# Performance work log

Measured on AMD Instinct MI355X. Metric: run time of the kernel, lower is better.

## Reference

```python
import jax, jax.numpy as jnp
from jax import lax
import numpy as np

WINDOW_SIZE = 11
SIGMA = 1.5
C1 = 0.01 ** 2
C2 = 0.03 ** 2


def _gauss_1d(n=WINDOW_SIZE, sigma=SIGMA):
    # replicates cv2.getGaussianKernel(n, sigma)
    x = np.arange(n, dtype=np.float64) - (n - 1) / 2.0
    g = np.exp(-(x ** 2) / (2.0 * sigma ** 2))
    return (g / g.sum()).astype(np.float32)


def _blur(x, g):
    """Separable 2D Gaussian blur of x [N,1,H,W]; math equals conv with g g^T."""
    p = g.shape[0] // 2
    kh = g.reshape(1, 1, -1, 1).astype(x.dtype)  # [O,I,KH,1]
    kw = g.reshape(1, 1, 1, -1).astype(x.dtype)  # [O,I,1,KW]
    dn = ('NCHW', 'OIHW', 'NCHW')
    x = lax.conv_general_dilated(x, kh, (1, 1), [(p, p), (0, 0)], dimension_numbers=dn)
    x = lax.conv_general_dilated(x, kw, (1, 1), [(0, 0), (p, p)], dimension_numbers=dn)
    return x


def _ssim_loss_2d(a, b):
    """a, b: [N,1,H,W]. Returns 1 - mean(SSIM map) with the module's exact formula."""
    g = jnp.asarray(_gauss_1d())
    mu1 = _blur(a, g)
    mu2 = _blur(b, g)
    mu1_sq = mu1 * mu1
    mu2_sq = mu2 * mu2
    mu1_mu2 = mu1 * mu2
    sigma1_sq = _blur(a * a, g) - mu1_sq
    sigma2_sq = _blur(b * b, g) - mu2_sq
    sigma12 = _blur(a * b, g) - mu1_mu2
    luminance = (2 * mu1_mu2 + C1) / (mu1_sq + mu2_sq + C1)
    contrast = (2 * sigma12 + C2) / (sigma1_sq + sigma2_sq + C2)
    structure = (sigma12 + C2) / (jnp.sqrt(sigma1_sq) * jnp.sqrt(sigma2_sq) + C2)
    ssim = luminance * contrast * structure
    return 1.0 - ssim.mean()


def setup_inputs() -> dict:
    key = jax.random.key(0)
    k1, k2, k3 = jax.random.split(key, 3)
    img1_3d = jax.random.uniform(k1, (4, 1, 16, 512, 512), dtype=jnp.float32)
    img1_2d = jax.random.uniform(k2, (4, 1, 512, 512), dtype=jnp.float32)
    img2 = jax.random.uniform(k3, (4, 1, 16, 512, 512), dtype=jnp.float32)
    return {"img1_3d": img1_3d, "img1_2d": img1_2d, "img2": img2}


def reference(img1_3d, img1_2d, img2):
    B, C, D, H, W = img1_3d.shape  # C == 1 (forced by groups=C with single-out-channel weight)
    # 3D SSIM: kernel depth 1, depth padding 0 -> per-slice 2D blur; fold D into batch.
    a3 = img1_3d.reshape(B * D, 1, H, W)
    b3 = img2.reshape(B * D, 1, H, W)
    loss3d = _ssim_loss_2d(a3, b3)
    # 2D SSIM against depth-averaged img2.
    b2 = jnp.mean(img2, axis=2)  # [B,1,H,W]
    loss2d = _ssim_loss_2d(img1_2d, b2)
    return loss3d + loss2d
```

## Files before the change

kernel.cpp:

```cpp
#include <hip/hip_runtime.h>
#include <cmath>


#define WSZ 11
#define IMG 512
#define SLICE (IMG * IMG)

typedef float f32x2 __attribute__((ext_vector_type(2)));
typedef float f32x4 __attribute__((ext_vector_type(4)));

struct G11 { float w[WSZ]; };

__device__ __forceinline__ void row_barrier()
{
    asm volatile("s_waitcnt lgkmcnt(0)" ::: "memory");
    __builtin_amdgcn_s_barrier();
}

__global__ __launch_bounds__(256, 4)
void ssim_pk_kernel(const float* __restrict__ A3, const float* __restrict__ B3,
                    const float* __restrict__ A2, const float* __restrict__ B2,
                    double* __restrict__ acc, G11 gw)
{
    __shared__ f32x4 A4[4][262];
    __shared__ f32x4 B4[4][262];
    __shared__ f32x2 Z2[4][262];
    __shared__ float bsum[4];

    const int tx = threadIdx.x;
    const int x0 = tx * 2;

    const int unit = blockIdx.x;
    const float* Ap;
    const float* Bp;
    double* accp;
    int y0, BAND;
    if (unit < 1024) {
        int slice = unit >> 4;
        int band  = unit & 15;
        Ap = A3 + (long)slice * SLICE;
        Bp = B3 + (long)slice * SLICE;
        accp = acc + 0;
        y0 = band * 32;
        BAND = 32;
    } else {
        int uu = unit - 1024;
        int img  = uu >> 6;
        int band = uu & 63;
        Ap = A2 + (long)img * SLICE;
        Bp = B2 + (long)img * SLICE;
        accp = acc + 1;
        y0 = band * 8;
        BAND = 8;
    }
    const int ITER = BAND >> 1;

    if (tx < 3) {
        f32x4 z4 = {0.f, 0.f, 0.f, 0.f};
        f32x2 z2 = {0.f, 0.f};
        #pragma unroll
        for (int b = 0; b < 4; b++) {
            A4[b][tx] = z4; A4[b][259 + tx] = z4;
            B4[b][tx] = z4; B4[b][259 + tx] = z4;
            Z2[b][tx] = z2; Z2[b][259 + tx] = z2;
        }
    }

    f32x2 ra[12], rb[12];

    float sum = 0.f;
    const f32x2 C1v = {1e-4f, 1e-4f};
    const f32x2 C2v = {9e-4f, 9e-4f};

    #pragma unroll
    for (int t = 0; t < 10; t++) {
        int r = y0 - 5 + t;
        f32x2 a = {0.f, 0.f}, b = {0.f, 0.f};
        if (r >= 0) {
            a = *(const f32x2*)&Ap[(long)r * IMG + x0];
            b = *(const f32x2*)&Bp[(long)r * IMG + x0];
        }
        ra[t] = a; rb[t] = b;
    }
    ra[10] = (f32x2){0.f, 0.f}; rb[10] = (f32x2){0.f, 0.f};
    ra[11] = (f32x2){0.f, 0.f}; rb[11] = (f32x2){0.f, 0.f};

    f32x2 aN0 = {0.f, 0.f}, bN0 = aN0, aN1 = aN0, bN1 = aN0;
    {
        int r0 = y0 + 5, r1 = y0 + 6;
        if (r0 < IMG) { aN0 = *(const f32x2*)&Ap[(long)r0 * IMG + x0];
                        bN0 = *(const f32x2*)&Bp[(long)r0 * IMG + x0]; }
        if (r1 < IMG) { aN1 = *(const f32x2*)&Ap[(long)r1 * IMG + x0];
                        bN1 = *(const f32x2*)&Bp[(long)r1 * IMG + x0]; }
    }

    auto vpass = [&](int base, int buf) {
        f32x2 m1 = {0.f, 0.f}, m2 = m1, xx = m1, yy = m1, zz = m1;
        #pragma unroll
        for (int j = 0; j < 11; j++) {
            const int s = (base + j) % 12;
            const f32x2 g2 = {gw.w[j], gw.w[j]};
            f32x2 a = ra[s], b = rb[s];
            f32x2 ga = g2 * a, gb = g2 * b;
            m1 += ga; m2 += gb;
            xx += ga * a; yy += gb * b; zz += ga * b;
        }
        A4[buf][3 + tx] = __builtin_shufflevector(m1, m2, 0, 1, 2, 3);
        B4[buf][3 + tx] = __builtin_shufflevector(xx, yy, 0, 1, 2, 3);
        Z2[buf][3 + tx] = zz;
    };

    auto hpass = [&](int buf) {
        f32x2 OM1 = {0.f, 0.f}, OM2 = OM1, OXX = OM1, OYY = OM1, OZZ = OM1;
        {
            f32x4 pa = A4[buf][tx], pb = B4[buf][tx];
            f32x2 pz = Z2[buf][tx];
            const f32x2 c = {gw.w[0], 0.f};
            OM1 += c * __builtin_shufflevector(pa, pa, 1, 1);
            OM2 += c * __builtin_shufflevector(pa, pa, 3, 3);
            OXX += c * __builtin_shufflevector(pb, pb, 1, 1);
            OYY += c * __builtin_shufflevector(pb, pb, 3, 3);
            OZZ += c * __builtin_shufflevector(pz, pz, 1, 1);
        }
        #pragma unroll
        for (int jj = 1; jj <= 5; jj++) {
            f32x4 pa = A4[buf][tx + jj], pb = B4[buf][tx + jj];
            f32x2 pz = Z2[buf][tx + jj];
            const f32x2 cA = {gw.w[2 * jj - 1], gw.w[2 * jj - 2]};
            const f32x2 cB = {gw.w[2 * jj],     gw.w[2 * jj - 1]};
            OM1 += cA * __builtin_shufflevector(pa, pa, 0, 0)
                 + cB * __builtin_shufflevector(pa, pa, 1, 1);
            OM2 += cA * __builtin_shufflevector(pa, pa, 2, 2)
                 + cB * __builtin_shufflevector(pa, pa, 3, 3);
            OXX += cA * __builtin_shufflevector(pb, pb, 0, 0)
                 + cB * __builtin_shufflevector(pb, pb, 1, 1);
            OYY += cA * __builtin_shufflevector(pb, pb, 2, 2)
                 + cB * __builtin_shufflevector(pb, pb, 3, 3);
            OZZ += cA * __builtin_shufflevector(pz, pz, 0, 0)
                 + cB * __builtin_shufflevector(pz, pz, 1, 1);
        }
        {
            f32x4 pa = A4[buf][tx + 6], pb = B4[buf][tx + 6];
            f32x2 pz = Z2[buf][tx + 6];
            const f32x2 c = {0.f, gw.w[10]};
            OM1 += c * __builtin_shufflevector(pa, pa, 0, 0);
            OM2 += c * __builtin_shufflevector(pa, pa, 2, 2);
            OXX += c * __builtin_shufflevector(pb, pb, 0, 0);
            OYY += c * __builtin_shufflevector(pb, pb, 2, 2);
            OZZ += c * __builtin_shufflevector(pz, pz, 0, 0);
        }
        f32x2 m1s = OM1 * OM1, m2s = OM2 * OM2, m12 = OM1 * OM2;
        f32x2 s1 = OXX - m1s, s2 = OYY - m2s, s12 = OZZ - m12;
        f32x2 d1 = m1s + m2s + C1v;
        f32x2 d2 = s1 + s2 + C2v;
        f32x2 num = (2.f * m12 + C1v) * (2.f * s12 + C2v) * (s12 + C2v);
        float d3x = __builtin_amdgcn_sqrtf(s1.x) * __builtin_amdgcn_sqrtf(s2.x) + 9e-4f;
        float d3y = __builtin_amdgcn_sqrtf(s1.y) * __builtin_amdgcn_sqrtf(s2.y) + 9e-4f;
        sum += num.x * __builtin_amdgcn_rcpf(d1.x * d2.x * d3x);
        sum += num.y * __builtin_amdgcn_rcpf(d1.y * d2.y * d3y);
    };

    for (int kk = 0; kk < ITER; kk += 6) {
        #pragma unroll
        for (int u = 0; u < 6; u++) {
            const int k = kk + u;
            if (k < ITER) {
                const int s0 = (10 + 2 * u) % 12;
                const int s1 = (11 + 2 * u) % 12;
                ra[s0] = aN0; rb[s0] = bN0;
                ra[s1] = aN1; rb[s1] = bN1;

                {
                    int r0 = y0 + 7 + 2 * k, r1 = r0 + 1;
                    aN0 = (f32x2){0.f, 0.f}; bN0 = aN0; aN1 = aN0; bN1 = aN0;
                    if (k + 1 < ITER) {
                        if (r0 < IMG) { aN0 = *(const f32x2*)&Ap[(long)r0 * IMG + x0];
                                        bN0 = *(const f32x2*)&Bp[(long)r0 * IMG + x0]; }
                        if (r1 < IMG) { aN1 = *(const f32x2*)&Ap[(long)r1 * IMG + x0];
                                        bN1 = *(const f32x2*)&Bp[(long)r1 * IMG + x0]; }
                    }
                }

                const int b0 = (u & 1) * 2;
                vpass(2 * u,     b0);
                vpass(2 * u + 1, b0 + 1);
                row_barrier();
                hpass(b0);
                hpass(b0 + 1);
            }
        }
    }

    for (int off = 32; off > 0; off >>= 1)
        sum += __shfl_down(sum, off, 64);
    if ((tx & 63) == 0) bsum[tx >> 6] = sum;
    __syncthreads();
    if (tx == 0) {
        float tot = bsum[0] + bsum[1] + bsum[2] + bsum[3];
        atomicAdd(accp, (double)tot);
    }
}

__global__ __launch_bounds__(256) void depth_mean4_kernel(
    const float4* __restrict__ img2, float4* __restrict__ b2)
{
    const int per = SLICE / 4;
    int idx = blockIdx.x * 256 + threadIdx.x;
    int b = idx >> 16;
    int p = idx & (per - 1);
    const float4* src = img2 + (long)b * 16 * per + p;
    float sx = 0.f, sy = 0.f, sz = 0.f, sw = 0.f;
    #pragma unroll
    for (int d = 0; d < 16; d++) {
        float4 v = src[(long)d * per];
        sx += v.x; sy += v.y; sz += v.z; sw += v.w;
    }
    float4 o; o.x = sx * 0.0625f; o.y = sy * 0.0625f; o.z = sz * 0.0625f; o.w = sw * 0.0625f;
    b2[idx] = o;
}

__global__ void finalize_kernel(const double* __restrict__ acc, float* __restrict__ out)
{
    double loss3 = 1.0 - acc[0] / (64.0 * (double)SLICE);
    double loss2 = 1.0 - acc[1] / (4.0 * (double)SLICE);
    out[0] = (float)(loss3 + loss2);
}

extern "C" void kernel_launch(void* const* d_in, const int* in_sizes, int n_in,
                              void* d_out, int out_size, void* d_ws, size_t ws_size,
                              hipStream_t stream)
{
    const float* img1_3d = (const float*)d_in[0];
    const float* img1_2d = (const float*)d_in[1];
    const float* img2    = (const float*)d_in[2];
    float* out = (float*)d_out;

    double* acc = (double*)d_ws;
    float*  b2  = (float*)((char*)d_ws + 256);

    G11 gw;
    {
        double g[WSZ], s = 0.0;
        for (int i = 0; i < WSZ; i++) {
            double xx = (double)i - (WSZ - 1) / 2.0;
            g[i] = std::exp(-(xx * xx) / (2.0 * 1.5 * 1.5));
            s += g[i];
        }
        for (int i = 0; i < WSZ; i++) gw.w[i] = (float)(g[i] / s);
    }

    hipMemsetAsync(acc, 0, 2 * sizeof(double), stream);

    depth_mean4_kernel<<<(4 * SLICE / 4) / 256, 256, 0, stream>>>(
        (const float4*)img2, (float4*)b2);

    ssim_pk_kernel<<<1280, 256, 0, stream>>>(img1_3d, img2, img1_2d, b2, acc, gw);

    finalize_kernel<<<1, 1, 0, stream>>>(acc, out);
}
```

Baseline: 95.28 us.

## Reorder separable blur to horizontal-first with register ring of vertical accumulators

The kernel now writes raw input rows (a,b) into shared memory and applies the horizontal blur first, computing squares and products on the fly. Each horizontal result is scattered into an 11-slot register ring of vertical accumulators, and a row's SSIM is evaluated once its accumulator is complete. This cuts shared-memory traffic from five blurred quantities to two raw values per pixel. In exchange it recomputes products per tap, adds halo rows to the loop, and raises register pressure, so the occupancy hint drops from 4 to 3.

```diff
diff --git a/kernel.cpp b/kernel.cpp
--- a/kernel.cpp
+++ b/kernel.cpp
@@ -17,14 +17,12 @@
     __builtin_amdgcn_s_barrier();
 }
 
-__global__ __launch_bounds__(256, 4)
-void ssim_pk_kernel(const float* __restrict__ A3, const float* __restrict__ B3,
+__global__ __launch_bounds__(256, 3)
+void ssim_hf_kernel(const float* __restrict__ A3, const float* __restrict__ B3,
                     const float* __restrict__ A2, const float* __restrict__ B2,
                     double* __restrict__ acc, G11 gw)
 {
-    __shared__ f32x4 A4[4][262];
-    __shared__ f32x4 B4[4][262];
-    __shared__ f32x2 Z2[4][262];
+    __shared__ f32x4 R4[4][262];
     __shared__ float bsum[4];
 
     const int tx = threadIdx.x;
@@ -53,140 +51,134 @@
         y0 = band * 8;
         BAND = 8;
     }
-    const int ITER = BAND >> 1;
+    const int NPAIR = (BAND + 10) >> 1;
 
     if (tx < 3) {
         f32x4 z4 = {0.f, 0.f, 0.f, 0.f};
-        f32x2 z2 = {0.f, 0.f};
-        #pragma unroll
-        for (int b = 0; b < 4; b++) {
-            A4[b][tx] = z4; A4[b][259 + tx] = z4;
-            B4[b][tx] = z4; B4[b][259 + tx] = z4;
-            Z2[b][tx] = z2; Z2[b][259 + tx] = z2;
-        }
-    }
-
-    f32x2 ra[12], rb[12];
+        #pragma unroll
+        for (int b = 0; b < 4; b++) { R4[b][tx] = z4; R4[b][259 + tx] = z4; }
+    }
+
+    f32x2 aM1[11], aM2[11], aXX[11], aYY[11], aZZ[11];
+    #pragma unroll
+    for (int i = 0; i < 11; i++) {
+        aM1[i] = (f32x2){0.f, 0.f}; aM2[i] = aM1[i]; aXX[i] = aM1[i];
+        aYY[i] = aM1[i]; aZZ[i] = aM1[i];
+    }
 
     float sum = 0.f;
     const f32x2 C1v = {1e-4f, 1e-4f};
     const f32x2 C2v = {9e-4f, 9e-4f};
 
-    #pragma unroll
-    for (int t = 0; t < 10; t++) {
-        int r = y0 - 5 + t;
-        f32x2 a = {0.f, 0.f}, b = {0.f, 0.f};
-        if (r >= 0) {
-            a = *(const f32x2*)&Ap[(long)r * IMG + x0];
-            b = *(const f32x2*)&Bp[(long)r * IMG + x0];
-        }
-        ra[t] = a; rb[t] = b;
-    }
-    ra[10] = (f32x2){0.f, 0.f}; rb[10] = (f32x2){0.f, 0.f};
-    ra[11] = (f32x2){0.f, 0.f}; rb[11] = (f32x2){0.f, 0.f};
-
     f32x2 aN0 = {0.f, 0.f}, bN0 = aN0, aN1 = aN0, bN1 = aN0;
     {
-        int r0 = y0 + 5, r1 = y0 + 6;
-        if (r0 < IMG) { aN0 = *(const f32x2*)&Ap[(long)r0 * IMG + x0];
-                        bN0 = *(const f32x2*)&Bp[(long)r0 * IMG + x0]; }
-        if (r1 < IMG) { aN1 = *(const f32x2*)&Ap[(long)r1 * IMG + x0];
-                        bN1 = *(const f32x2*)&Bp[(long)r1 * IMG + x0]; }
-    }
-
-    auto vpass = [&](int base, int buf) {
-        f32x2 m1 = {0.f, 0.f}, m2 = m1, xx = m1, yy = m1, zz = m1;
-        #pragma unroll
-        for (int j = 0; j < 11; j++) {
-            const int s = (base + j) % 12;
-            const f32x2 g2 = {gw.w[j], gw.w[j]};
-            f32x2 a = ra[s], b = rb[s];
-            f32x2 ga = g2 * a, gb = g2 * b;
-            m1 += ga; m2 += gb;
-            xx += ga * a; yy += gb * b; zz += ga * b;
-        }
-        A4[buf][3 + tx] = __builtin_shufflevector(m1, m2, 0, 1, 2, 3);
-        B4[buf][3 + tx] = __builtin_shufflevector(xx, yy, 0, 1, 2, 3);
-        Z2[buf][3 + tx] = zz;
-    };
-
-    auto hpass = [&](int buf) {
-        f32x2 OM1 = {0.f, 0.f}, OM2 = OM1, OXX = OM1, OYY = OM1, OZZ = OM1;
+        int r0 = y0 - 5, r1 = y0 - 4;
+        if (r0 >= 0 && r0 < IMG) { aN0 = *(const f32x2*)&Ap[(long)r0 * IMG + x0];
+                                   bN0 = *(const f32x2*)&Bp[(long)r0 * IMG + x0]; }
+        if (r1 >= 0 && r1 < IMG) { aN1 = *(const f32x2*)&Ap[(long)r1 * IMG + x0];
+                                   bN1 = *(const f32x2*)&Bp[(long)r1 * IMG + x0]; }
+    }
+
+    auto PROC = [&](int set, int u2, bool complete) {
+        f32x2 H1 = {0.f, 0.f}, H2 = H1, H3 = H1, H4 = H1, H5 = H1;
         {
-            f32x4 pa = A4[buf][tx], pb = B4[buf][tx];
-            f32x2 pz = Z2[buf][tx];
+            f32x4 p = R4[set][tx];
+            f32x4 q = p * p;
+            f32x2 ab = __builtin_shufflevector(p, p, 0, 1)
+                     * __builtin_shufflevector(p, p, 2, 3);
             const f32x2 c = {gw.w[0], 0.f};
-            OM1 += c * __builtin_shufflevector(pa, pa, 1, 1);
-            OM2 += c * __builtin_shufflevector(pa, pa, 3, 3);
-            OXX += c * __builtin_shufflevector(pb, pb, 1, 1);
-            OYY += c * __builtin_shufflevector(pb, pb, 3, 3);
-            OZZ += c * __builtin_shufflevector(pz, pz, 1, 1);
+            H1 += c * __builtin_shufflevector(p, p, 1, 1);
+            H2 += c * __builtin_shufflevector(p, p, 3, 3);
+            H3 += c * __builtin_shufflevector(q, q, 1, 1);
+            H4 += c * __builtin_shufflevector(q, q, 3, 3);
+            H5 += c * __builtin_shufflevector(ab, ab, 1, 1);
         }
         #pragma unroll
         for (int jj = 1; jj <= 5; jj++) {
-            f32x4 pa = A4[buf][tx + jj], pb = B4[buf][tx + jj];
-            f32x2 pz = Z2[buf][tx + jj];
+            f32x4 p = R4[set][tx + jj];
+            f32x4 q = p * p;
+            f32x2 ab = __builtin_shufflevector(p, p, 0, 1)
+                     * __builtin_shufflevector(p, p, 2, 3);
             const f32x2 cA = {gw.w[2 * jj - 1], gw.w[2 * jj - 2]};
             const f32x2 cB = {gw.w[2 * jj],     gw.w[2 * jj - 1]};
-            OM1 += cA * __builtin_shufflevector(pa, pa, 0, 0)
-                 + cB * __builtin_shufflevector(pa, pa, 1, 1);
-            OM2 += cA * __builtin_shufflevector(pa, pa, 2, 2)
-                 + cB * __builtin_shufflevector(pa, pa, 3, 3);
-            OXX += cA * __builtin_shufflevector(pb, pb, 0, 0)
-                 + cB * __builtin_shufflevector(pb, pb, 1, 1);
-            OYY += cA * __builtin_shufflevector(pb, pb, 2, 2)
-                 + cB * __builtin_shufflevector(pb, pb, 3, 3);
-            OZZ += cA * __builtin_shufflevector(pz, pz, 0, 0)
-                 + cB * __builtin_shufflevector(pz, pz, 1, 1);
+            H1 += cA * __builtin_shufflevector(p, p, 0, 0)
+                + cB * __builtin_shufflevector(p, p, 1, 1);
+            H2 += cA * __builtin_shufflevector(p, p, 2, 2)
+                + cB * __builtin_shufflevector(p, p, 3, 3);
+            H3 += cA * __builtin_shufflevector(q, q, 0, 0)
+                + cB * __builtin_shufflevector(q, q, 1, 1);
+            H4 += cA * __builtin_shufflevector(q, q, 2, 2)
+                + cB * __builtin_shufflevector(q, q, 3, 3);
+            H5 += cA * __builtin_shufflevector(ab, ab, 0, 0)
+                + cB * __builtin_shufflevector(ab, ab, 1, 1);
         }
         {
-            f32x4 pa = A4[buf][tx + 6], pb = B4[buf][tx + 6];
-            f32x2 pz = Z2[buf][tx + 6];
+            f32x4 p = R4[set][tx + 6];
+            f32x4 q = p * p;
+            f32x2 ab = __builtin_shufflevector(p, p, 0, 1)
+                     * __builtin_shufflevector(p, p, 2, 3);
             const f32x2 c = {0.f, gw.w[10]};
-            OM1 += c * __builtin_shufflevector(pa, pa, 0, 0);
-            OM2 += c * __builtin_shufflevector(pa, pa, 2, 2);
-            OXX += c * __builtin_shufflevector(pb, pb, 0, 0);
-            OYY += c * __builtin_shufflevector(pb, pb, 2, 2);
-            OZZ += c * __builtin_shufflevector(pz, pz, 0, 0);
-        }
-        f32x2 m1s = OM1 * OM1, m2s = OM2 * OM2, m12 = OM1 * OM2;
-        f32x2 s1 = OXX - m1s, s2 = OYY - m2s, s12 = OZZ - m12;
-        f32x2 d1 = m1s + m2s + C1v;
-        f32x2 d2 = s1 + s2 + C2v;
-        f32x2 num = (2.f * m12 + C1v) * (2.f * s12 + C2v) * (s12 + C2v);
-        float d3x = __builtin_amdgcn_sqrtf(s1.x) * __builtin_amdgcn_sqrtf(s2.x) + 9e-4f;
-        float d3y = __builtin_amdgcn_sqrtf(s1.y) * __builtin_amdgcn_sqrtf(s2.y) + 9e-4f;
-        sum += num.x * __builtin_amdgcn_rcpf(d1.x * d2.x * d3x);
-        sum += num.y * __builtin_amdgcn_rcpf(d1.y * d2.y * d3y);
+            H1 += c * __builtin_shufflevector(p, p, 0, 0);
+            H2 += c * __builtin_shufflevector(p, p, 2, 2);
+            H3 += c * __builtin_shufflevector(q, q, 0, 0);
+            H4 += c * __builtin_shufflevector(q, q, 2, 2);
+            H5 += c * __builtin_shufflevector(ab, ab, 0, 0);
+        }
+
+        #pragma unroll
+        for (int j = 0; j < 11; j++) {
+            const int s = (u2 + j) % 11;
+            const f32x2 gj = {gw.w[10 - j], gw.w[10 - j]};
+            aM1[s] += gj * H1; aM2[s] += gj * H2;
+            aXX[s] += gj * H3; aYY[s] += gj * H4; aZZ[s] += gj * H5;
+        }
+
+        if (complete) {
+            f32x2 M1 = aM1[u2], M2 = aM2[u2];
+            f32x2 XX = aXX[u2], YY = aYY[u2], ZZ = aZZ[u2];
+            f32x2 m1s = M1 * M1, m2s = M2 * M2, m12 = M1 * M2;
+            f32x2 s1 = XX - m1s, s2 = YY - m2s, s12 = ZZ - m12;
+            f32x2 d1 = m1s + m2s + C1v;
+            f32x2 d2 = s1 + s2 + C2v;
+            f32x2 num = (2.f * m12 + C1v) * (2.f * s12 + C2v) * (s12 + C2v);
+            float d3x = __builtin_amdgcn_sqrtf(s1.x) * __builtin_amdgcn_sqrtf(s2.x) + 9e-4f;
+            float d3y = __builtin_amdgcn_sqrtf(s1.y) * __builtin_amdgcn_sqrtf(s2.y) + 9e-4f;
+            sum += num.x * __builtin_amdgcn_rcpf(d1.x * d2.x * d3x);
+            sum += num.y * __builtin_amdgcn_rcpf(d1.y * d2.y * d3y);
+        }
+        aM1[u2] = (f32x2){0.f, 0.f}; aM2[u2] = aM1[u2];
+        aXX[u2] = aM1[u2]; aYY[u2] = aM1[u2]; aZZ[u2] = aM1[u2];
     };
 
-    for (int kk = 0; kk < ITER; kk += 6) {
-        #pragma unroll
-        for (int u = 0; u < 6; u++) {
+    for (int kk = 0; kk < NPAIR; kk += 11) {
+        #pragma unroll
+        for (int u = 0; u < 11; u++) {
             const int k = kk + u;
-            if (k < ITER) {
-                const int s0 = (10 + 2 * u) % 12;
-                const int s1 = (11 + 2 * u) % 12;
-                ra[s0] = aN0; rb[s0] = bN0;
-                ra[s1] = aN1; rb[s1] = bN1;
+            if (k < NPAIR) {
+                const int b0 = (u & 1) * 2;
+                R4[b0    ][3 + tx] = (f32x4){aN0.x, aN0.y, bN0.x, bN0.y};
+                R4[b0 + 1][3 + tx] = (f32x4){aN1.x, aN1.y, bN1.x, bN1.y};
 
                 {
-                    int r0 = y0 + 7 + 2 * k, r1 = r0 + 1;
+                    int r0 = y0 - 5 + 2 * (k + 1), r1 = r0 + 1;
                     aN0 = (f32x2){0.f, 0.f}; bN0 = aN0; aN1 = aN0; bN1 = aN0;
-                    if (k + 1 < ITER) {
-                        if (r0 < IMG) { aN0 = *(const f32x2*)&Ap[(long)r0 * IMG + x0];
-                                        bN0 = *(const f32x2*)&Bp[(long)r0 * IMG + x0]; }
-                        if (r1 < IMG) { aN1 = *(const f32x2*)&Ap[(long)r1 * IMG + x0];
-                                        bN1 = *(const f32x2*)&Bp[(long)r1 * IMG + x0]; }
+                    if (k + 1 < NPAIR) {
+                        if (r0 >= 0 && r0 < IMG) {
+                            aN0 = *(const f32x2*)&Ap[(long)r0 * IMG + x0];
+                            bN0 = *(const f32x2*)&Bp[(long)r0 * IMG + x0];
+                        }
+                        if (r1 >= 0 && r1 < IMG) {
+                            aN1 = *(const f32x2*)&Ap[(long)r1 * IMG + x0];
+                            bN1 = *(const f32x2*)&Bp[(long)r1 * IMG + x0];
+                        }
                     }
                 }
 
-                const int b0 = (u & 1) * 2;
-                vpass(2 * u,     b0);
-                vpass(2 * u + 1, b0 + 1);
                 row_barrier();
-                hpass(b0);
-                hpass(b0 + 1);
+
+                const bool done = (k >= 5);
+                PROC(b0,     (2 * u)     % 11, done);
+                PROC(b0 + 1, (2 * u + 1) % 11, done);
             }
         }
     }
@@ -254,7 +246,7 @@
     depth_mean4_kernel<<<(4 * SLICE / 4) / 256, 256, 0, stream>>>(
         (const float4*)img2, (float4*)b2);
 
-    ssim_pk_kernel<<<1280, 256, 0, stream>>>(img1_3d, img2, img1_2d, b2, acc, gw);
+    ssim_hf_kernel<<<1280, 256, 0, stream>>>(img1_3d, img2, img1_2d, b2, acc, gw);
 
     finalize_kernel<<<1, 1, 0, stream>>>(acc, out);
 }
```

Result: slower. 102.1 us (+7.2%).
